# Kernel optimization log

Measured on AMD Instinct MI355X. Metric: run time of the kernel, lower is better.

The kernel has to match this reference:

```python
import jax, jax.numpy as jnp
import numpy as np

B, S, D = 2, 2048, 2048
H = 16
HD = D // H            # 128 head dim
L = 512                # latent dim
R = 64                 # rope dim (min(64, HD) = 64)
RH = R // 2
SCALE = HD ** -0.5     # note: uses head_dim, not head_dim+rope_dim
NEG = jnp.float32(-1e9)


def _rope_tables():
    inv_freq = 1.0 / (10000.0 ** (jnp.arange(0, R, 2, dtype=jnp.float32) / R))  # [RH]
    pos = jnp.arange(S, dtype=jnp.float32)
    freqs = pos[:, None] * inv_freq[None, :]  # [S, RH]
    return jnp.cos(freqs), jnp.sin(freqs)


def _apply_rope(x, cos, sin):
    # x: [B, H, S, R], interleaved even/odd rotation as in the torch source
    xe, xo = x[..., 0::2], x[..., 1::2]                    # [B,H,S,RH]
    c = cos[None, None]
    s = sin[None, None]
    re = xe * c - xo * s
    ro = xe * s + xo * c
    return jnp.stack([re, ro], axis=-1).reshape(x.shape)   # re-interleave


def setup_inputs() -> dict:
    key = jax.random.key(0)
    ks = jax.random.split(key, 8)
    std = 0.02
    f32 = jnp.float32
    return {
        "x":     jax.random.normal(ks[0], (B, S, D), f32),
        "W_ckv": jax.random.normal(ks[1], (D, L), f32) * std,      # compress_kv
        "W_kv":  jax.random.normal(ks[2], (L, 2 * D), f32) * std,  # kv_proj
        "W_cq":  jax.random.normal(ks[3], (D, L), f32) * std,      # compress_q
        "W_q":   jax.random.normal(ks[4], (L, D), f32) * std,      # q_proj
        "W_qr":  jax.random.normal(ks[5], (L, H * R), f32) * std,  # q_rope
        "W_kr":  jax.random.normal(ks[6], (L, R), f32) * std,      # k_rope
        "W_out": jax.random.normal(ks[7], (D, D), f32) * std,      # out_proj
    }


def reference(x, W_ckv, W_kv, W_cq, W_q, W_qr, W_kr, W_out):
    cos, sin = _rope_tables()

    c_kv = x @ W_ckv                                   # [B,S,L]
    kv = c_kv @ W_kv                                   # [B,S,2D]
    c_q = x @ W_cq                                     # [B,S,L]

    q_c = (c_q @ W_q).reshape(B, S, H, HD).transpose(0, 2, 1, 3)    # [B,H,S,HD]
    q_r = (c_q @ W_qr).reshape(B, S, H, R).transpose(0, 2, 1, 3)    # [B,H,S,R]
    k_r = (c_kv @ W_kr)[:, None, :, :]                               # [B,1,S,R]

    k_c, v = jnp.split(kv, 2, axis=-1)
    k_c = k_c.reshape(B, S, H, HD).transpose(0, 2, 1, 3)             # [B,H,S,HD]
    v = v.reshape(B, S, H, HD).transpose(0, 2, 1, 3)                 # [B,H,S,HD]

    q_r = _apply_rope(q_r, cos, sin)
    k_r = jnp.broadcast_to(_apply_rope(k_r, cos, sin), (B, H, S, R))

    q = jnp.concatenate([q_c, q_r], axis=-1)                         # [B,H,S,HD+R]
    k = jnp.concatenate([k_c, k_r], axis=-1)                         # [B,H,S,HD+R]

    scores = jnp.einsum("bhqd,bhkd->bhqk", q, k) * SCALE             # [B,H,S,S]
    causal = jnp.tril(jnp.ones((S, S), dtype=bool))
    scores = jnp.where(causal[None, None], scores, NEG)
    p = jax.nn.softmax(scores, axis=-1)
    attended = jnp.einsum("bhqk,bhkd->bhqd", p, v)                   # [B,H,S,HD]

    out = attended.transpose(0, 2, 1, 3).reshape(B, S, D) @ W_out    # [B,S,D]
    return out  # dropout is identity in eval / p=0
```

## Files before the change

### kernel.cpp

```cpp
#include <hip/hip_runtime.h>
#include <hip/hip_bf16.h>
#include <cstdint>
#include <cstddef>

typedef __bf16 bf16;
typedef __attribute__((ext_vector_type(2))) __bf16 bf16x2;
typedef __attribute__((ext_vector_type(4))) __bf16 bf16x4;
typedef __attribute__((ext_vector_type(8))) __bf16 bf16x8;
typedef __attribute__((ext_vector_type(4))) float f32x4;

#define MFMA16(a, b, c) __builtin_amdgcn_mfma_f32_16x16x32_bf16((a), (b), (c), 0, 0, 0)
#define SCALE_L2E 0.127517432f

#define QCR_STRIDE 3072
#define KV_STRIDE  4160

__device__ __forceinline__ void gload16(const void* g, void* l) {
    __builtin_amdgcn_global_load_lds(
        (const __attribute__((address_space(1))) void*)g,
        (__attribute__((address_space(3))) void*)l, 16, 0, 0);
}

__device__ __forceinline__ void bar_lgkm() {
    asm volatile("s_waitcnt lgkmcnt(0)" ::: "memory");
    __builtin_amdgcn_s_barrier();
    asm volatile("" ::: "memory");
}

__device__ __forceinline__ int pack_bf16(float a, float b) {
    bf16x2 p; p[0] = (bf16)a; p[1] = (bf16)b;
    return __builtin_bit_cast(int, p);
}

__global__ __launch_bounds__(256) void k_cvtAll(
    const float* __restrict__ w_ckv, const float* __restrict__ w_kv,
    const float* __restrict__ w_cq, const float* __restrict__ w_q,
    const float* __restrict__ w_qr, const float* __restrict__ w_kr,
    bf16* __restrict__ WCT, bf16* __restrict__ WKVKRT, bf16* __restrict__ WQQRT,
    const float* __restrict__ x, bf16* __restrict__ XB)
{
    __shared__ float tile[32][33];
    int bid = blockIdx.x;
    const int t = threadIdx.x;
    if (bid >= 5664) {
        int n4 = (4096 * 2048) / 4;
        int i = (bid - 5664) * 256 + t;
        int stride = 2048 * 256;
        const float4* in4 = (const float4*)x;
        bf16x4* o4 = (bf16x4*)XB;
        for (; i < n4; i += stride) {
            float4 v = in4[i];
            bf16x4 o;
            o[0] = (bf16)v.x; o[1] = (bf16)v.y; o[2] = (bf16)v.z; o[3] = (bf16)v.w;
            o4[i] = o;
        }
        return;
    }
    const float* src; bf16* dst; int Kd, Nd, loc;
    if (bid < 1024)      { src = w_ckv; dst = WCT;                   Kd = 2048; Nd = 512;  loc = bid; }
    else if (bid < 3072) { src = w_kv;  dst = WKVKRT;                Kd = 512;  Nd = 4096; loc = bid - 1024; }
    else if (bid < 4096) { src = w_cq;  dst = WCT + 512ull * 2048;   Kd = 2048; Nd = 512;  loc = bid - 3072; }
    else if (bid < 5120) { src = w_q;   dst = WQQRT;                 Kd = 512;  Nd = 2048; loc = bid - 4096; }
    else if (bid < 5632) { src = w_qr;  dst = WQQRT + 2048ull * 512; Kd = 512;  Nd = 1024; loc = bid - 5120; }
    else                 { src = w_kr;  dst = WKVKRT + 4096ull * 512; Kd = 512; Nd = 64;   loc = bid - 5632; }
    const int nbx = Nd / 32;
    const int n0 = (loc % nbx) * 32, k0 = (loc / nbx) * 32;
    const int r = t >> 3, c4 = (t & 7) * 4;
    float4 v = *(const float4*)(src + (size_t)(k0 + r) * Nd + n0 + c4);
    tile[r][c4 + 0] = v.x; tile[r][c4 + 1] = v.y;
    tile[r][c4 + 2] = v.z; tile[r][c4 + 3] = v.w;
    __syncthreads();
    bf16x4 o;
    o[0] = (bf16)tile[c4 + 0][r]; o[1] = (bf16)tile[c4 + 1][r];
    o[2] = (bf16)tile[c4 + 2][r]; o[3] = (bf16)tile[c4 + 3][r];
    *(bf16x4*)(dst + (size_t)(n0 + r) * Kd + k0 + c4) = o;
}

__global__ __launch_bounds__(256) void k_cvtT(const float* __restrict__ in,
                                              bf16* __restrict__ out, int Kd, int Nd)
{
    __shared__ float tile[32][33];
    const int k0 = blockIdx.y * 32, n0 = blockIdx.x * 32;
    const int t = threadIdx.x;
    const int r = t >> 3, c4 = (t & 7) * 4;
    float4 v = *(const float4*)(in + (size_t)(k0 + r) * Nd + n0 + c4);
    tile[r][c4 + 0] = v.x; tile[r][c4 + 1] = v.y;
    tile[r][c4 + 2] = v.z; tile[r][c4 + 3] = v.w;
    __syncthreads();
    bf16x4 o;
    o[0] = (bf16)tile[c4 + 0][r]; o[1] = (bf16)tile[c4 + 1][r];
    o[2] = (bf16)tile[c4 + 2][r]; o[3] = (bf16)tile[c4 + 3][r];
    *(bf16x4*)(out + (size_t)(n0 + r) * Kd + k0 + c4) = o;
}

template<int MF, int NF, bool F32OUT, bool ROPE>
__device__ __forceinline__ void gemm_body(
    const bf16* __restrict__ A, const bf16* __restrict__ BT,
    bf16* __restrict__ Cb, float* __restrict__ Cf,
    int M, int N, int K, int lda, float cscale, int ropeStart, int bx, int by,
    bf16* As, bf16* Bs)
{
    constexpr int ASTR = MF * 1024, BSTR = NF * 1024;
    const int t = threadIdx.x;
    const int m0 = by * (MF * 32);
    const int n0 = bx * (NF * 32);
    const int wid = t >> 6, lane = t & 63;
    const int wm = (wid >> 1) * (MF * 16), wn = (wid & 1) * (NF * 16);
    const int lr = lane & 15, lk = (lane >> 4) * 8;

    const int srow = t >> 2, skc = (t & 3) << 3;
    const int bn0 = min(n0 + srow, N - 1);
    const int bn1 = min(n0 + srow + 64, N - 1);

    f32x4 acc[MF][NF];
    const f32x4 z = {0.f, 0.f, 0.f, 0.f};
#pragma unroll
    for (int m = 0; m < MF; ++m)
#pragma unroll
        for (int n = 0; n < NF; ++n) acc[m][n] = z;

    auto stage = [&](int buf, int k0) {
        gload16(BT + (size_t)bn0 * K + k0 + skc, Bs + buf * BSTR + t * 8);
        if constexpr (NF == 4)
            gload16(BT + (size_t)bn1 * K + k0 + skc, Bs + buf * BSTR + (t + 256) * 8);
        gload16(A + (size_t)(m0 + srow) * lda + k0 + skc, As + buf * ASTR + t * 8);
        if constexpr (MF == 4)
            gload16(A + (size_t)(m0 + srow + 64) * lda + k0 + skc, As + buf * ASTR + (t + 256) * 8);
    };

    stage(0, 0);
    __syncthreads();

    for (int k0 = 0; k0 < K; k0 += 32) {
        const int cur = (k0 >> 5) & 1;
        if (k0 + 32 < K) stage(cur ^ 1, k0 + 32);

        bf16x8 af[MF], bfr[NF];
#pragma unroll
        for (int m = 0; m < MF; ++m)
            af[m] = *(const bf16x8*)(As + cur * ASTR + (wm + m * 16 + lr) * 32 + lk);
#pragma unroll
        for (int n = 0; n < NF; ++n)
            bfr[n] = *(const bf16x8*)(Bs + cur * BSTR + (wn + n * 16 + lr) * 32 + lk);
#pragma unroll
        for (int m = 0; m < MF; ++m)
#pragma unroll
            for (int n = 0; n < NF; ++n)
                acc[m][n] = MFMA16(af[m], bfr[n], acc[m][n]);

        __syncthreads();
    }

    const int lrow4 = (lane >> 4) * 4;
#pragma unroll
    for (int m = 0; m < MF; ++m)
#pragma unroll
        for (int n = 0; n < NF; ++n)
#pragma unroll
            for (int i = 0; i < 4; ++i) {
                int r = m0 + wm + m * 16 + lrow4 + i;
                int c = n0 + wn + n * 16 + lr;
                float val = acc[m][n][i] * cscale;
                if constexpr (ROPE) {
                    float part = __shfl_xor(val, 1, 64);
                    if (c >= ropeStart) {
                        int i2 = ((c - ropeStart) & 63) >> 1;
                        int s = r & 2047;
                        float ang = (float)s * __expf(-(float)i2 * 0.28782313662f);
                        float sn, cs;
                        __sincosf(ang, &sn, &cs);
                        val = (c & 1) ? (part * sn + val * cs)
                                      : (val * cs - part * sn);
                    }
                }
                if (r < M && c < N) {
                    if constexpr (F32OUT) Cf[(size_t)r * N + c] = val;
                    else Cb[(size_t)r * N + c] = (bf16)val;
                }
            }
}

template<int MF, int NF, bool F32OUT>
__global__ __launch_bounds__(256) void k_gemm_bt(
    const bf16* __restrict__ A, const bf16* __restrict__ BT,
    bf16* __restrict__ Cb, float* __restrict__ Cf,
    int M, int N, int K, int lda, float cscale)
{
    __shared__ bf16 As[2 * MF * 1024];
    __shared__ bf16 Bs[2 * NF * 1024];
    gemm_body<MF, NF, F32OUT, false>(A, BT, Cb, Cf, M, N, K, lda, cscale, 1 << 30,
                                     blockIdx.x, blockIdx.y, As, Bs);
}

__global__ __launch_bounds__(256) void k_gemm_dual(
    const bf16* __restrict__ C, const bf16* __restrict__ WKVKRT,
    const bf16* __restrict__ WQQRT, bf16* __restrict__ KVKR, bf16* __restrict__ QCR)
{
    __shared__ bf16 As[2 * 4096];
    __shared__ bf16 Bs[2 * 4096];
    int bid = blockIdx.x;
    if (bid < 1056) {
        gemm_body<4, 4, false, true>(C, WKVKRT, KVKR, nullptr, 4096, 4160, 512, 1024,
                                     1.0f, 4096, bid % 33, bid / 33, As, Bs);
    } else {
        bid -= 1056;
        gemm_body<4, 4, false, true>(C + 512, WQQRT, QCR, nullptr, 4096, 3072, 512, 1024,
                                     SCALE_L2E, 2048, bid % 24, bid / 24, As, Bs);
    }
}

__global__ __launch_bounds__(256, 3) void k_attn(
    const bf16* __restrict__ qcr, const bf16* __restrict__ kvkr,
    bf16* __restrict__ att)
{
    __shared__ bf16 Ksc[64 * 128];
    __shared__ bf16 Ksr[64 * 64];
    __shared__ bf16 Vt[128 * 64];

    const int L = blockIdx.x;
    const int qt = 31 - (L >> 5);
    const int bh = L & 31;
    const int h = bh & 15, b = bh >> 4;

    const int t = threadIdx.x;
    const int wid = t >> 6, lane = t & 63;
    const int lr = lane & 15, lq = lane >> 4, lk = lq * 8;
    const size_t rowbase = (size_t)b * 2048;

    const f32x4 z = {0.f, 0.f, 0.f, 0.f};

    auto rho = [](int r) {
        return (((r >> 5) & 1) << 5) | (((r >> 2) & 1) << 4) | (((r >> 3) & 3) << 2) | (r & 3);
    };

    const int vk = (t & 31) * 2;
    const int vf = (t >> 5) * 8;

    bf16x8 rc[4], rr[2], rv[4];
    auto LOAD = [&](int kb) {
#pragma unroll
        for (int i = 0; i < 4; ++i) {
            int bb = t + 256 * i;
            int row = bb >> 4, gcb = bb & 15;
            rc[i] = *(const bf16x8*)(kvkr + (rowbase + kb + row) * KV_STRIDE + h * 128 + gcb * 8);
        }
#pragma unroll
        for (int i = 0; i < 2; ++i) {
            int bb = t + 256 * i;
            int row = bb >> 3, gcb = bb & 7;
            rr[i] = *(const bf16x8*)(kvkr + (rowbase + kb + row) * KV_STRIDE + 4096 + gcb * 8);
        }
#pragma unroll
        for (int i = 0; i < 2; ++i) {
            const bf16* vs = kvkr + (rowbase + kb + vk) * KV_STRIDE + 2048 + h * 128 + vf + 64 * i;
            rv[2 * i]     = *(const bf16x8*)vs;
            rv[2 * i + 1] = *(const bf16x8*)(vs + KV_STRIDE);
        }
    };
    auto WRITE = [&]() {
#pragma unroll
        for (int i = 0; i < 4; ++i) {
            int bb = t + 256 * i;
            int row = rho(bb >> 4), gcb = bb & 15;
            int scb = (gcb & 8) | ((gcb ^ row) & 7);
            *(bf16x8*)(Ksc + row * 128 + scb * 8) = rc[i];
        }
#pragma unroll
        for (int i = 0; i < 2; ++i) {
            int bb = t + 256 * i;
            int row = rho(bb >> 3), gcb = bb & 7;
            int scb = (gcb ^ row) & 7;
            *(bf16x8*)(Ksr + row * 64 + scb * 8) = rr[i];
        }
#pragma unroll
        for (int i = 0; i < 2; ++i)
#pragma unroll
            for (int j = 0; j < 8; ++j) {
                int feat = vf + 64 * i + j;
                int scb = ((vk >> 3) ^ (feat & 7)) & 7;
                bf16x2 pr; pr[0] = rv[2 * i][j]; pr[1] = rv[2 * i + 1][j];
                *(bf16x2*)(Vt + feat * 64 + scb * 8 + (vk & 7)) = pr;
            }
    };

    const int qrow_w = qt * 64 + wid * 16;
    const int qi = qrow_w + lr;

    bf16x8 qf[6];
    {
        const size_t qrow = rowbase + qi;
        const bf16* qp = qcr + qrow * QCR_STRIDE + h * 128;
#pragma unroll
        for (int ks = 0; ks < 4; ++ks) qf[ks] = *(const bf16x8*)(qp + ks * 32 + lk);
        const bf16* qp2 = qcr + qrow * QCR_STRIDE + 2048 + h * 64;
#pragma unroll
        for (int ks = 0; ks < 2; ++ks) qf[4 + ks] = *(const bf16x8*)(qp2 + ks * 32 + lk);
    }

    float mrow = -3e38f, lsum = 0.f;
    f32x4 o[8];
#pragma unroll
    for (int n = 0; n < 8; ++n) o[n] = z;

    const int nkt = qt + 1;
    LOAD(0);

#pragma unroll 1
    for (int kt = 0; kt < nkt; ++kt) {
        const int kb = kt * 64;
        bar_lgkm();
        WRITE();
        if (kt + 1 < nkt) LOAD(kb + 64);
        bar_lgkm();

        if (kb > qrow_w + 15) continue;

        f32x4 sacc[4];
        __builtin_amdgcn_s_setprio(1);
#pragma unroll
        for (int kg = 0; kg < 4; ++kg) {
            f32x4 s = z;
            const int key = kg * 16 + lr;
#pragma unroll
            for (int ks = 0; ks < 4; ++ks) {
                int cb = ks * 4 + lq;
                int scb = (cb & 8) | ((cb ^ key) & 7);
                bf16x8 kf = *(const bf16x8*)(Ksc + key * 128 + scb * 8);
                s = MFMA16(kf, qf[ks], s);
            }
#pragma unroll
            for (int ks = 0; ks < 2; ++ks) {
                int cb = ks * 4 + lq;
                int scb = (cb ^ key) & 7;
                bf16x8 kf = *(const bf16x8*)(Ksr + key * 64 + scb * 8);
                s = MFMA16(kf, qf[4 + ks], s);
            }
            sacc[kg] = s;
        }
        __builtin_amdgcn_s_setprio(0);

        const bool domask = (kb + 63) > qrow_w;
        if (domask) {
#pragma unroll
            for (int kg = 0; kg < 4; ++kg) {
                int keybase = kb + ((kg >> 1) << 5) + (lq << 3) + ((kg & 1) << 2);
#pragma unroll
                for (int i = 0; i < 4; ++i)
                    if (keybase + i > qi) sacc[kg][i] = -3e38f;
            }
        }

        f32x4 mv;
#pragma unroll
        for (int i = 0; i < 4; ++i)
            mv[i] = fmaxf(fmaxf(sacc[0][i], sacc[1][i]), fmaxf(sacc[2][i], sacc[3][i]));
        float mx = fmaxf(fmaxf(mv[0], mv[1]), fmaxf(mv[2], mv[3]));
        mx = fmaxf(mx, __shfl_xor(mx, 16, 64));
        mx = fmaxf(mx, __shfl_xor(mx, 32, 64));

        if (__any(mx > mrow)) {
            float mnew = fmaxf(mrow, mx);
            float scl = __builtin_amdgcn_exp2f(mrow - mnew);
            mrow = mnew;
            lsum *= scl;
#pragma unroll
            for (int n = 0; n < 8; ++n)
#pragma unroll
                for (int i = 0; i < 4; ++i) o[n][i] *= scl;
        }

        f32x4 sv = z;
#pragma unroll
        for (int kg = 0; kg < 4; ++kg)
#pragma unroll
            for (int i = 0; i < 4; ++i) {
                float pv = __builtin_amdgcn_exp2f(sacc[kg][i] - mrow);
                sacc[kg][i] = pv;
                sv[i] += pv;
            }
        float rs = (sv[0] + sv[1]) + (sv[2] + sv[3]);
        rs += __shfl_xor(rs, 16, 64);
        rs += __shfl_xor(rs, 32, 64);
        lsum += rs;

        __builtin_amdgcn_s_setprio(1);
#pragma unroll
        for (int s = 0; s < 2; ++s) {
            union { int4 iv; bf16x8 v; } pb;
            pb.iv.x = pack_bf16(sacc[2 * s][0], sacc[2 * s][1]);
            pb.iv.y = pack_bf16(sacc[2 * s][2], sacc[2 * s][3]);
            pb.iv.z = pack_bf16(sacc[2 * s + 1][0], sacc[2 * s + 1][1]);
            pb.iv.w = pack_bf16(sacc[2 * s + 1][2], sacc[2 * s + 1][3]);
#pragma unroll
            for (int n = 0; n < 8; ++n) {
                int feat = n * 16 + lr;
                int scb = ((s * 4 + lq) ^ (feat & 7)) & 7;
                bf16x8 vfr = *(const bf16x8*)(Vt + feat * 64 + scb * 8);
                o[n] = MFMA16(vfr, pb.v, o[n]);
            }
        }
        __builtin_amdgcn_s_setprio(0);
    }

    const float inv = 1.f / lsum;
    const size_t orow = (rowbase + qi) * 2048 + h * 128;
#pragma unroll
    for (int n = 0; n < 8; ++n) {
        bf16x4 ov;
#pragma unroll
        for (int i = 0; i < 4; ++i) ov[i] = (bf16)(o[n][i] * inv);
        *(bf16x4*)(att + orow + n * 16 + (lq << 2)) = ov;
    }
}

extern "C" void kernel_launch(void* const* d_in, const int* in_sizes, int n_in,
                              void* d_out, int out_size, void* d_ws, size_t ws_size,
                              hipStream_t stream)
{
    (void)in_sizes; (void)n_in; (void)out_size; (void)ws_size;
    const float* x = (const float*)d_in[0];
    const float* w_ckv = (const float*)d_in[1];
    const float* w_kv = (const float*)d_in[2];
    const float* w_cq = (const float*)d_in[3];
    const float* w_q = (const float*)d_in[4];
    const float* w_qr = (const float*)d_in[5];
    const float* w_kr = (const float*)d_in[6];
    const float* w_out = (const float*)d_in[7];
    float* out = (float*)d_out;

    char* ws = (char*)d_ws;
    size_t off = 0;
    auto take = [&](size_t elems) -> bf16* {
        bf16* p = (bf16*)(ws + off);
        off += (elems * sizeof(bf16) + 255) & ~(size_t)255;
        return p;
    };
    bf16* WCT    = take(1024ull * 2048);
    bf16* WKVKRT = take(4160ull * 512);
    bf16* WQQRT  = take(3072ull * 512);
    bf16* C      = take(4096ull * 1024);
    bf16* KVKR   = take(4096ull * 4160);
    bf16* QCR    = take(4096ull * 3072);
    bf16* ATT    = take(4096ull * 2048);
    bf16* WOUTT  = C;
    bf16* XB     = KVKR;

    k_cvtAll<<<7712, 256, 0, stream>>>(w_ckv, w_kv, w_cq, w_q, w_qr, w_kr,
                                       WCT, WKVKRT, WQQRT, x, XB);

    k_gemm_bt<4, 2, false><<<dim3(16, 32), 256, 0, stream>>>(
        XB, WCT, C, nullptr, 4096, 1024, 2048, 2048, 1.0f);

    k_gemm_dual<<<1824, 256, 0, stream>>>(C, WKVKRT, WQQRT, KVKR, QCR);

    k_cvtT<<<dim3(64, 64), 256, 0, stream>>>(w_out, WOUTT, 2048, 2048);

    k_attn<<<1024, 256, 0, stream>>>(QCR, KVKR, ATT);

    k_gemm_bt<2, 4, true><<<dim3(16, 64), 256, 0, stream>>>(
        ATT, WOUTT, nullptr, out, 4096, 2048, 2048, 2048, 1.0f);
}
```

Before: 248.4 us.

## Double query rows per attention block to reuse K/V tiles across two fragments

Each attention block now handles 128 query rows (each wave 32 rows as two 16-row fragments) instead of 64, so every K and V fragment read from shared memory feeds two MFMAs. This halves the K/V global loads and LDS staging per query row, and the grid shrinks from 1024 to 512 blocks. The costs are higher register pressure (launch bounds drop from 3 to 2 waves per SIMD), fewer blocks to balance the causal workload, and more masked wasted work on diagonal tiles.

```diff
diff --git a/kernel.cpp b/kernel.cpp
--- a/kernel.cpp
+++ b/kernel.cpp
@@ -209,7 +209,7 @@
     }
 }
 
-__global__ __launch_bounds__(256, 3) void k_attn(
+__global__ __launch_bounds__(256, 2) void k_attn(
     const bf16* __restrict__ qcr, const bf16* __restrict__ kvkr,
     bf16* __restrict__ att)
 {
@@ -218,7 +218,7 @@
     __shared__ bf16 Vt[128 * 64];
 
     const int L = blockIdx.x;
-    const int qt = 31 - (L >> 5);
+    const int qt = 15 - (L >> 5);
     const int bh = L & 31;
     const int h = bh & 15, b = bh >> 4;
 
@@ -283,26 +283,31 @@
             }
     };
 
-    const int qrow_w = qt * 64 + wid * 16;
-    const int qi = qrow_w + lr;
-
-    bf16x8 qf[6];
-    {
-        const size_t qrow = rowbase + qi;
+    const int qrow_w = qt * 128 + wid * 32;
+    const int qi0 = qrow_w + lr;
+    const int qi1 = qrow_w + 16 + lr;
+
+    bf16x8 qf[2][6];
+#pragma unroll
+    for (int f = 0; f < 2; ++f) {
+        const size_t qrow = rowbase + qrow_w + f * 16 + lr;
         const bf16* qp = qcr + qrow * QCR_STRIDE + h * 128;
 #pragma unroll
-        for (int ks = 0; ks < 4; ++ks) qf[ks] = *(const bf16x8*)(qp + ks * 32 + lk);
+        for (int ks = 0; ks < 4; ++ks) qf[f][ks] = *(const bf16x8*)(qp + ks * 32 + lk);
         const bf16* qp2 = qcr + qrow * QCR_STRIDE + 2048 + h * 64;
 #pragma unroll
-        for (int ks = 0; ks < 2; ++ks) qf[4 + ks] = *(const bf16x8*)(qp2 + ks * 32 + lk);
-    }
-
-    float mrow = -3e38f, lsum = 0.f;
-    f32x4 o[8];
-#pragma unroll
-    for (int n = 0; n < 8; ++n) o[n] = z;
-
-    const int nkt = qt + 1;
+        for (int ks = 0; ks < 2; ++ks) qf[f][4 + ks] = *(const bf16x8*)(qp2 + ks * 32 + lk);
+    }
+
+    float mrow0 = -3e38f, lsum0 = 0.f;
+    float mrow1 = -3e38f, lsum1 = 0.f;
+    f32x4 o[2][8];
+#pragma unroll
+    for (int f = 0; f < 2; ++f)
+#pragma unroll
+        for (int n = 0; n < 8; ++n) o[f][n] = z;
+
+    const int nkt = 2 * qt + 2;
     LOAD(0);
 
 #pragma unroll 1
@@ -313,29 +318,31 @@
         if (kt + 1 < nkt) LOAD(kb + 64);
         bar_lgkm();
 
-        if (kb > qrow_w + 15) continue;
-
-        f32x4 sacc[4];
+        if (kb > qrow_w + 31) continue;
+
+        f32x4 sacc0[4], sacc1[4];
         __builtin_amdgcn_s_setprio(1);
 #pragma unroll
         for (int kg = 0; kg < 4; ++kg) {
-            f32x4 s = z;
+            f32x4 s0 = z, s1 = z;
             const int key = kg * 16 + lr;
 #pragma unroll
             for (int ks = 0; ks < 4; ++ks) {
                 int cb = ks * 4 + lq;
                 int scb = (cb & 8) | ((cb ^ key) & 7);
                 bf16x8 kf = *(const bf16x8*)(Ksc + key * 128 + scb * 8);
-                s = MFMA16(kf, qf[ks], s);
+                s0 = MFMA16(kf, qf[0][ks], s0);
+                s1 = MFMA16(kf, qf[1][ks], s1);
             }
 #pragma unroll
             for (int ks = 0; ks < 2; ++ks) {
                 int cb = ks * 4 + lq;
                 int scb = (cb ^ key) & 7;
                 bf16x8 kf = *(const bf16x8*)(Ksr + key * 64 + scb * 8);
-                s = MFMA16(kf, qf[4 + ks], s);
-            }
-            sacc[kg] = s;
+                s0 = MFMA16(kf, qf[0][4 + ks], s0);
+                s1 = MFMA16(kf, qf[1][4 + ks], s1);
+            }
+            sacc0[kg] = s0; sacc1[kg] = s1;
         }
         __builtin_amdgcn_s_setprio(0);
 
@@ -345,71 +352,101 @@
             for (int kg = 0; kg < 4; ++kg) {
                 int keybase = kb + ((kg >> 1) << 5) + (lq << 3) + ((kg & 1) << 2);
 #pragma unroll
-                for (int i = 0; i < 4; ++i)
-                    if (keybase + i > qi) sacc[kg][i] = -3e38f;
-            }
-        }
-
-        f32x4 mv;
-#pragma unroll
-        for (int i = 0; i < 4; ++i)
-            mv[i] = fmaxf(fmaxf(sacc[0][i], sacc[1][i]), fmaxf(sacc[2][i], sacc[3][i]));
-        float mx = fmaxf(fmaxf(mv[0], mv[1]), fmaxf(mv[2], mv[3]));
-        mx = fmaxf(mx, __shfl_xor(mx, 16, 64));
-        mx = fmaxf(mx, __shfl_xor(mx, 32, 64));
-
-        if (__any(mx > mrow)) {
-            float mnew = fmaxf(mrow, mx);
-            float scl = __builtin_amdgcn_exp2f(mrow - mnew);
-            mrow = mnew;
-            lsum *= scl;
+                for (int i = 0; i < 4; ++i) {
+                    if (keybase + i > qi0) sacc0[kg][i] = -3e38f;
+                    if (keybase + i > qi1) sacc1[kg][i] = -3e38f;
+                }
+            }
+        }
+
+        float mx0, mx1;
+        {
+            f32x4 mv0, mv1;
+#pragma unroll
+            for (int i = 0; i < 4; ++i) {
+                mv0[i] = fmaxf(fmaxf(sacc0[0][i], sacc0[1][i]), fmaxf(sacc0[2][i], sacc0[3][i]));
+                mv1[i] = fmaxf(fmaxf(sacc1[0][i], sacc1[1][i]), fmaxf(sacc1[2][i], sacc1[3][i]));
+            }
+            mx0 = fmaxf(fmaxf(mv0[0], mv0[1]), fmaxf(mv0[2], mv0[3]));
+            mx1 = fmaxf(fmaxf(mv1[0], mv1[1]), fmaxf(mv1[2], mv1[3]));
+            mx0 = fmaxf(mx0, __shfl_xor(mx0, 16, 64));
+            mx0 = fmaxf(mx0, __shfl_xor(mx0, 32, 64));
+            mx1 = fmaxf(mx1, __shfl_xor(mx1, 16, 64));
+            mx1 = fmaxf(mx1, __shfl_xor(mx1, 32, 64));
+        }
+
+        if (__any((mx0 > mrow0) | (mx1 > mrow1))) {
+            float mnew0 = fmaxf(mrow0, mx0);
+            float mnew1 = fmaxf(mrow1, mx1);
+            float scl0 = __builtin_amdgcn_exp2f(mrow0 - mnew0);
+            float scl1 = __builtin_amdgcn_exp2f(mrow1 - mnew1);
+            mrow0 = mnew0; mrow1 = mnew1;
+            lsum0 *= scl0; lsum1 *= scl1;
 #pragma unroll
             for (int n = 0; n < 8; ++n)
 #pragma unroll
-                for (int i = 0; i < 4; ++i) o[n][i] *= scl;
-        }
-
-        f32x4 sv = z;
+                for (int i = 0; i < 4; ++i) {
+                    o[0][n][i] *= scl0;
+                    o[1][n][i] *= scl1;
+                }
+        }
+
+        f32x4 sv0 = z, sv1 = z;
 #pragma unroll
         for (int kg = 0; kg < 4; ++kg)
 #pragma unroll
             for (int i = 0; i < 4; ++i) {
-                float pv = __builtin_amdgcn_exp2f(sacc[kg][i] - mrow);
-                sacc[kg][i] = pv;
-                sv[i] += pv;
-            }
-        float rs = (sv[0] + sv[1]) + (sv[2] + sv[3]);
-        rs += __shfl_xor(rs, 16, 64);
-        rs += __shfl_xor(rs, 32, 64);
-        lsum += rs;
+                float p0 = __builtin_amdgcn_exp2f(sacc0[kg][i] - mrow0);
+                float p1 = __builtin_amdgcn_exp2f(sacc1[kg][i] - mrow1);
+                sacc0[kg][i] = p0; sacc1[kg][i] = p1;
+                sv0[i] += p0; sv1[i] += p1;
+            }
+        float rs0 = (sv0[0] + sv0[1]) + (sv0[2] + sv0[3]);
+        float rs1 = (sv1[0] + sv1[1]) + (sv1[2] + sv1[3]);
+        rs0 += __shfl_xor(rs0, 16, 64);
+        rs0 += __shfl_xor(rs0, 32, 64);
+        rs1 += __shfl_xor(rs1, 16, 64);
+        rs1 += __shfl_xor(rs1, 32, 64);
+        lsum0 += rs0; lsum1 += rs1;
 
         __builtin_amdgcn_s_setprio(1);
 #pragma unroll
         for (int s = 0; s < 2; ++s) {
-            union { int4 iv; bf16x8 v; } pb;
-            pb.iv.x = pack_bf16(sacc[2 * s][0], sacc[2 * s][1]);
-            pb.iv.y = pack_bf16(sacc[2 * s][2], sacc[2 * s][3]);
-            pb.iv.z = pack_bf16(sacc[2 * s + 1][0], sacc[2 * s + 1][1]);
-            pb.iv.w = pack_bf16(sacc[2 * s + 1][2], sacc[2 * s + 1][3]);
+            union { int4 iv; bf16x8 v; } pb0, pb1;
+            pb0.iv.x = pack_bf16(sacc0[2 * s][0], sacc0[2 * s][1]);
+            pb0.iv.y = pack_bf16(sacc0[2 * s][2], sacc0[2 * s][3]);
+            pb0.iv.z = pack_bf16(sacc0[2 * s + 1][0], sacc0[2 * s + 1][1]);
+            pb0.iv.w = pack_bf16(sacc0[2 * s + 1][2], sacc0[2 * s + 1][3]);
+            pb1.iv.x = pack_bf16(sacc1[2 * s][0], sacc1[2 * s][1]);
+            pb1.iv.y = pack_bf16(sacc1[2 * s][2], sacc1[2 * s][3]);
+            pb1.iv.z = pack_bf16(sacc1[2 * s + 1][0], sacc1[2 * s + 1][1]);
+            pb1.iv.w = pack_bf16(sacc1[2 * s + 1][2], sacc1[2 * s + 1][3]);
 #pragma unroll
             for (int n = 0; n < 8; ++n) {
                 int feat = n * 16 + lr;
                 int scb = ((s * 4 + lq) ^ (feat & 7)) & 7;
                 bf16x8 vfr = *(const bf16x8*)(Vt + feat * 64 + scb * 8);
-                o[n] = MFMA16(vfr, pb.v, o[n]);
+                o[0][n] = MFMA16(vfr, pb0.v, o[0][n]);
+                o[1][n] = MFMA16(vfr, pb1.v, o[1][n]);
             }
         }
         __builtin_amdgcn_s_setprio(0);
     }
 
-    const float inv = 1.f / lsum;
-    const size_t orow = (rowbase + qi) * 2048 + h * 128;
+    const float inv0 = 1.f / lsum0;
+    const float inv1 = 1.f / lsum1;
+    const size_t orow0 = (rowbase + qi0) * 2048 + h * 128;
+    const size_t orow1 = (rowbase + qi1) * 2048 + h * 128;
 #pragma unroll
     for (int n = 0; n < 8; ++n) {
-        bf16x4 ov;
-#pragma unroll
-        for (int i = 0; i < 4; ++i) ov[i] = (bf16)(o[n][i] * inv);
-        *(bf16x4*)(att + orow + n * 16 + (lq << 2)) = ov;
+        bf16x4 ov0, ov1;
+#pragma unroll
+        for (int i = 0; i < 4; ++i) {
+            ov0[i] = (bf16)(o[0][n][i] * inv0);
+            ov1[i] = (bf16)(o[1][n][i] * inv1);
+        }
+        *(bf16x4*)(att + orow0 + n * 16 + (lq << 2)) = ov0;
+        *(bf16x4*)(att + orow1 + n * 16 + (lq << 2)) = ov1;
     }
 }
 
@@ -455,7 +492,7 @@
 
     k_cvtT<<<dim3(64, 64), 256, 0, stream>>>(w_out, WOUTT, 2048, 2048);
 
-    k_attn<<<1024, 256, 0, stream>>>(QCR, KVKR, ATT);
+    k_attn<<<512, 256, 0, stream>>>(QCR, KVKR, ATT);
 
     k_gemm_bt<2, 4, true><<<dim3(16, 64), 256, 0, stream>>>(
         ATT, WOUTT, nullptr, out, 4096, 2048, 2048, 2048, 1.0f);
```

New measurement: 265.1 us. 1.07x slower.

## Double-buffer K/V tiles in attention kernel to drop one barrier per iteration

Applied to the files above, without the earlier changes.

The attention kernel now keeps two LDS buffers for the K-content, K-rope and transposed V tiles. Each iteration computes on the current buffer, then writes the prefetched registers into the other buffer and issues the next global load, so only one barrier per key tile is needed instead of two. This doubles LDS use per block from 48KB to 96KB, which may cut how many blocks fit on a CU alongside the launch bound of 3.

```diff
diff --git a/kernel.cpp b/kernel.cpp
--- a/kernel.cpp
+++ b/kernel.cpp
@@ -213,9 +213,9 @@
     const bf16* __restrict__ qcr, const bf16* __restrict__ kvkr,
     bf16* __restrict__ att)
 {
-    __shared__ bf16 Ksc[64 * 128];
-    __shared__ bf16 Ksr[64 * 64];
-    __shared__ bf16 Vt[128 * 64];
+    __shared__ bf16 Ksc[2][64 * 128];
+    __shared__ bf16 Ksr[2][64 * 64];
+    __shared__ bf16 Vt[2][128 * 64];
 
     const int L = blockIdx.x;
     const int qt = 31 - (L >> 5);
@@ -257,20 +257,20 @@
             rv[2 * i + 1] = *(const bf16x8*)(vs + KV_STRIDE);
         }
     };
-    auto WRITE = [&]() {
+    auto WRITE = [&](int bf) {
 #pragma unroll
         for (int i = 0; i < 4; ++i) {
             int bb = t + 256 * i;
             int row = rho(bb >> 4), gcb = bb & 15;
             int scb = (gcb & 8) | ((gcb ^ row) & 7);
-            *(bf16x8*)(Ksc + row * 128 + scb * 8) = rc[i];
+            *(bf16x8*)(&Ksc[bf][row * 128 + scb * 8]) = rc[i];
         }
 #pragma unroll
         for (int i = 0; i < 2; ++i) {
             int bb = t + 256 * i;
             int row = rho(bb >> 3), gcb = bb & 7;
             int scb = (gcb ^ row) & 7;
-            *(bf16x8*)(Ksr + row * 64 + scb * 8) = rr[i];
+            *(bf16x8*)(&Ksr[bf][row * 64 + scb * 8]) = rr[i];
         }
 #pragma unroll
         for (int i = 0; i < 2; ++i)
@@ -279,7 +279,7 @@
                 int feat = vf + 64 * i + j;
                 int scb = ((vk >> 3) ^ (feat & 7)) & 7;
                 bf16x2 pr; pr[0] = rv[2 * i][j]; pr[1] = rv[2 * i + 1][j];
-                *(bf16x2*)(Vt + feat * 64 + scb * 8 + (vk & 7)) = pr;
+                *(bf16x2*)(&Vt[bf][feat * 64 + scb * 8 + (vk & 7)]) = pr;
             }
     };
 
@@ -304,102 +304,108 @@
 
     const int nkt = qt + 1;
     LOAD(0);
+    WRITE(0);
+    if (nkt > 1) LOAD(64);
+    bar_lgkm();
 
 #pragma unroll 1
     for (int kt = 0; kt < nkt; ++kt) {
         const int kb = kt * 64;
+        const int cur = kt & 1;
+
+        if (kb <= qrow_w + 15) {
+            f32x4 sacc[4];
+            __builtin_amdgcn_s_setprio(1);
+#pragma unroll
+            for (int kg = 0; kg < 4; ++kg) {
+                f32x4 s = z;
+                const int key = kg * 16 + lr;
+#pragma unroll
+                for (int ks = 0; ks < 4; ++ks) {
+                    int cb = ks * 4 + lq;
+                    int scb = (cb & 8) | ((cb ^ key) & 7);
+                    bf16x8 kf = *(const bf16x8*)(&Ksc[cur][key * 128 + scb * 8]);
+                    s = MFMA16(kf, qf[ks], s);
+                }
+#pragma unroll
+                for (int ks = 0; ks < 2; ++ks) {
+                    int cb = ks * 4 + lq;
+                    int scb = (cb ^ key) & 7;
+                    bf16x8 kf = *(const bf16x8*)(&Ksr[cur][key * 64 + scb * 8]);
+                    s = MFMA16(kf, qf[4 + ks], s);
+                }
+                sacc[kg] = s;
+            }
+            __builtin_amdgcn_s_setprio(0);
+
+            const bool domask = (kb + 63) > qrow_w;
+            if (domask) {
+#pragma unroll
+                for (int kg = 0; kg < 4; ++kg) {
+                    int keybase = kb + ((kg >> 1) << 5) + (lq << 3) + ((kg & 1) << 2);
+#pragma unroll
+                    for (int i = 0; i < 4; ++i)
+                        if (keybase + i > qi) sacc[kg][i] = -3e38f;
+                }
+            }
+
+            f32x4 mv;
+#pragma unroll
+            for (int i = 0; i < 4; ++i)
+                mv[i] = fmaxf(fmaxf(sacc[0][i], sacc[1][i]), fmaxf(sacc[2][i], sacc[3][i]));
+            float mx = fmaxf(fmaxf(mv[0], mv[1]), fmaxf(mv[2], mv[3]));
+            mx = fmaxf(mx, __shfl_xor(mx, 16, 64));
+            mx = fmaxf(mx, __shfl_xor(mx, 32, 64));
+
+            if (__any(mx > mrow)) {
+                float mnew = fmaxf(mrow, mx);
+                float scl = __builtin_amdgcn_exp2f(mrow - mnew);
+                mrow = mnew;
+                lsum *= scl;
+#pragma unroll
+                for (int n = 0; n < 8; ++n)
+#pragma unroll
+                    for (int i = 0; i < 4; ++i) o[n][i] *= scl;
+            }
+
+            f32x4 sv = z;
+#pragma unroll
+            for (int kg = 0; kg < 4; ++kg)
+#pragma unroll
+                for (int i = 0; i < 4; ++i) {
+                    float pv = __builtin_amdgcn_exp2f(sacc[kg][i] - mrow);
+                    sacc[kg][i] = pv;
+                    sv[i] += pv;
+                }
+            float rs = (sv[0] + sv[1]) + (sv[2] + sv[3]);
+            rs += __shfl_xor(rs, 16, 64);
+            rs += __shfl_xor(rs, 32, 64);
+            lsum += rs;
+
+            __builtin_amdgcn_s_setprio(1);
+#pragma unroll
+            for (int s = 0; s < 2; ++s) {
+                union { int4 iv; bf16x8 v; } pb;
+                pb.iv.x = pack_bf16(sacc[2 * s][0], sacc[2 * s][1]);
+                pb.iv.y = pack_bf16(sacc[2 * s][2], sacc[2 * s][3]);
+                pb.iv.z = pack_bf16(sacc[2 * s + 1][0], sacc[2 * s + 1][1]);
+                pb.iv.w = pack_bf16(sacc[2 * s + 1][2], sacc[2 * s + 1][3]);
+#pragma unroll
+                for (int n = 0; n < 8; ++n) {
+                    int feat = n * 16 + lr;
+                    int scb = ((s * 4 + lq) ^ (feat & 7)) & 7;
+                    bf16x8 vfr = *(const bf16x8*)(&Vt[cur][feat * 64 + scb * 8]);
+                    o[n] = MFMA16(vfr, pb.v, o[n]);
+                }
+            }
+            __builtin_amdgcn_s_setprio(0);
+        }
+
+        if (kt + 1 < nkt) {
+            WRITE(cur ^ 1);
+            if (kt + 2 < nkt) LOAD(kb + 128);
+        }
         bar_lgkm();
-        WRITE();
-        if (kt + 1 < nkt) LOAD(kb + 64);
-        bar_lgkm();
-
-        if (kb > qrow_w + 15) continue;
-
-        f32x4 sacc[4];
-        __builtin_amdgcn_s_setprio(1);
-#pragma unroll
-        for (int kg = 0; kg < 4; ++kg) {
-            f32x4 s = z;
-            const int key = kg * 16 + lr;
-#pragma unroll
-            for (int ks = 0; ks < 4; ++ks) {
-                int cb = ks * 4 + lq;
-                int scb = (cb & 8) | ((cb ^ key) & 7);
-                bf16x8 kf = *(const bf16x8*)(Ksc + key * 128 + scb * 8);
-                s = MFMA16(kf, qf[ks], s);
-            }
-#pragma unroll
-            for (int ks = 0; ks < 2; ++ks) {
-                int cb = ks * 4 + lq;
-                int scb = (cb ^ key) & 7;
-                bf16x8 kf = *(const bf16x8*)(Ksr + key * 64 + scb * 8);
-                s = MFMA16(kf, qf[4 + ks], s);
-            }
-            sacc[kg] = s;
-        }
-        __builtin_amdgcn_s_setprio(0);
-
-        const bool domask = (kb + 63) > qrow_w;
-        if (domask) {
-#pragma unroll
-            for (int kg = 0; kg < 4; ++kg) {
-                int keybase = kb + ((kg >> 1) << 5) + (lq << 3) + ((kg & 1) << 2);
-#pragma unroll
-                for (int i = 0; i < 4; ++i)
-                    if (keybase + i > qi) sacc[kg][i] = -3e38f;
-            }
-        }
-
-        f32x4 mv;
-#pragma unroll
-        for (int i = 0; i < 4; ++i)
-            mv[i] = fmaxf(fmaxf(sacc[0][i], sacc[1][i]), fmaxf(sacc[2][i], sacc[3][i]));
-        float mx = fmaxf(fmaxf(mv[0], mv[1]), fmaxf(mv[2], mv[3]));
-        mx = fmaxf(mx, __shfl_xor(mx, 16, 64));
-        mx = fmaxf(mx, __shfl_xor(mx, 32, 64));
-
-        if (__any(mx > mrow)) {
-            float mnew = fmaxf(mrow, mx);
-            float scl = __builtin_amdgcn_exp2f(mrow - mnew);
-            mrow = mnew;
-            lsum *= scl;
-#pragma unroll
-            for (int n = 0; n < 8; ++n)
-#pragma unroll
-                for (int i = 0; i < 4; ++i) o[n][i] *= scl;
-        }
-
-        f32x4 sv = z;
-#pragma unroll
-        for (int kg = 0; kg < 4; ++kg)
-#pragma unroll
-            for (int i = 0; i < 4; ++i) {
-                float pv = __builtin_amdgcn_exp2f(sacc[kg][i] - mrow);
-                sacc[kg][i] = pv;
-                sv[i] += pv;
-            }
-        float rs = (sv[0] + sv[1]) + (sv[2] + sv[3]);
-        rs += __shfl_xor(rs, 16, 64);
-        rs += __shfl_xor(rs, 32, 64);
-        lsum += rs;
-
-        __builtin_amdgcn_s_setprio(1);
-#pragma unroll
-        for (int s = 0; s < 2; ++s) {
-            union { int4 iv; bf16x8 v; } pb;
-            pb.iv.x = pack_bf16(sacc[2 * s][0], sacc[2 * s][1]);
-            pb.iv.y = pack_bf16(sacc[2 * s][2], sacc[2 * s][3]);
-            pb.iv.z = pack_bf16(sacc[2 * s + 1][0], sacc[2 * s + 1][1]);
-            pb.iv.w = pack_bf16(sacc[2 * s + 1][2], sacc[2 * s + 1][3]);
-#pragma unroll
-            for (int n = 0; n < 8; ++n) {
-                int feat = n * 16 + lr;
-                int scb = ((s * 4 + lq) ^ (feat & 7)) & 7;
-                bf16x8 vfr = *(const bf16x8*)(Vt + feat * 64 + scb * 8);
-                o[n] = MFMA16(vfr, pb.v, o[n]);
-            }
-        }
-        __builtin_amdgcn_s_setprio(0);
     }
 
     const float inv = 1.f / lsum;
```

Result: no change. 247.5 us (-0.4%).
